# Optimization experiments

Hardware: AMD Instinct MI355X
Metric: run time of the kernel (lower is better)

Reference implementation:

```python
import jax, jax.numpy as jnp
import numpy as np

B, N, C, H, R = 64, 197, 768, 12, 98   # batch, tokens, dim, heads, eliminated tokens
SPARSITY, ALPHA = 0.2, 0.1
EPS = 1e-5  # torch nn.LayerNorm default


def layernorm(x, g, b):
    m = jnp.mean(x, axis=-1, keepdims=True)
    v = jnp.var(x, axis=-1, keepdims=True)
    return (x - m) / jnp.sqrt(v + EPS) * g + b


def setup_inputs() -> dict:
    key = jax.random.key(0)
    ks = jax.random.split(key, 8)
    s = lambda k, sh: (jax.random.normal(k, sh, jnp.float32) * 0.02)
    return dict(
        x=jax.random.normal(ks[0], (B, N, C), jnp.float32),
        norm1_g=jnp.ones((C,), jnp.float32), norm1_b=jnp.zeros((C,), jnp.float32),
        qkv_w=s(ks[1], (C, 3 * C)),                      # qkv_bias=False
        proj_w=s(ks[2], (C, C)), proj_b=jnp.zeros((C,), jnp.float32),
        norm2_g=jnp.ones((C,), jnp.float32), norm2_b=jnp.zeros((C,), jnp.float32),
        fc1_w=s(ks[3], (C, 4 * C)), fc1_b=jnp.zeros((4 * C,), jnp.float32),
        fc2_w=s(ks[4], (4 * C, C)), fc2_b=jnp.zeros((C,), jnp.float32),
    )


def reference(x, norm1_g, norm1_b, qkv_w, proj_w, proj_b,
              norm2_g, norm2_b, fc1_w, fc1_b, fc2_w, fc2_b):
    Dh = C // H
    scale = Dh ** -0.5
    # --- attention block ---
    h = layernorm(x, norm1_g, norm1_b)
    qkv = (h @ qkv_w).reshape(B, N, 3, H, Dh).transpose(2, 0, 3, 1, 4)
    q, k, v = qkv[0] * scale, qkv[1], qkv[2]
    attn = jax.nn.softmax(jnp.einsum('bhnd,bhmd->bhnm', q, k), axis=-1)  # [B,H,N,N]
    out = jnp.einsum('bhnm,bhmd->bhnd', attn, v).transpose(0, 2, 1, 3).reshape(B, N, C)
    x = x + out @ proj_w + proj_b
    # --- selection: DiagAttn (head-mean attention diagonal, excluding CLS) ---
    diag = jnp.diagonal(attn.mean(1), axis1=1, axis2=2)[:, 1:]          # [B, N-1]
    token_rank = jnp.argsort(-diag, axis=1) + 1                          # indices into [1, N)
    nk = N - 1 - R                                                       # kept image tokens
    idx_kept = jnp.sort(jnp.concatenate(
        [jnp.zeros((B, 1), token_rank.dtype), token_rank[:, :nk]], axis=1), axis=1)  # [B, K]
    idx_elim = jnp.sort(token_rank[:, nk:], axis=1)                      # [B, R]
    K = nk + 1
    # --- propagate: ThresholdGraph (multihead=True, threshold=True) ---
    x_kept = jnp.take_along_axis(x, idx_kept[:, :, None], axis=1)        # [B, K, C]
    x_elim = jnp.take_along_axis(x, idx_elim[:, :, None], axis=1)        # [B, R, C]
    w = jnp.take_along_axis(attn, idx_kept[:, None, :, None], axis=2)    # [B,H,K,N]
    w = jnp.take_along_axis(w, idx_elim[:, None, None, :], axis=3)       # [B,H,K,R]
    thr_idx = int(R * K * SPARSITY)
    w_sorted = -jnp.sort(-w.reshape(B, H, K * R), axis=-1)               # descending
    thr = w_sorted[:, :, thr_idx][:, :, None, None]
    w = jnp.where(w >= thr, w, jnp.zeros((), w.dtype))
    x_prop = jnp.einsum('bhke,behd->bkhd', w, x_elim.reshape(B, R, H, Dh)).reshape(B, K, C)
    x = x_kept + ALPHA * x_prop                                          # [B, K, C]
    # --- mlp block ---
    h2 = layernorm(x, norm2_g, norm2_b)
    h2 = jax.nn.gelu(h2 @ fc1_w + fc1_b, approximate=False) @ fc2_w + fc2_b
    return x + h2
```

## Files before the change

### kernel.cpp

```cpp
#include <hip/hip_runtime.h>
#include <math.h>

#define NTOK 197
#define CD   768
#define NH   12
#define DH   64
#define NBATCH 64
#define RTOK 98
#define KTOK 99
#define THRN 1941
#define WTOT (KTOK*RTOK)
#define SROWS 208

typedef __attribute__((ext_vector_type(8))) short short8;
typedef __attribute__((ext_vector_type(8))) unsigned short u16x8;
typedef __attribute__((ext_vector_type(4))) float floatx4;

__device__ __forceinline__ int clamp196(int v){ return ((unsigned)v > 196u) ? 196 : v; }
__device__ __forceinline__ unsigned short f2b(float f){
  unsigned u = __float_as_uint(f);
  return (unsigned short)((u + 0x7FFFu + ((u>>16)&1u)) >> 16);
}
__device__ __forceinline__ float us2f(unsigned short u){ return __uint_as_float(((unsigned)u)<<16); }
__device__ __forceinline__ int swz(int row, int q){ return q ^ (((row>>1)&3)<<3); }

__device__ __forceinline__ void ldsplit(const float* ap, int rem, u16x8& h, u16x8& l){
  float v[8];
  if (rem >= 8) {
    float4 t0 = *(const float4*)ap, t1 = *(const float4*)(ap+4);
    v[0]=t0.x; v[1]=t0.y; v[2]=t0.z; v[3]=t0.w;
    v[4]=t1.x; v[5]=t1.y; v[6]=t1.z; v[7]=t1.w;
  } else {
#pragma unroll
    for (int j=0;j<8;j++) v[j] = (j < rem) ? ap[j] : 0.f;
  }
#pragma unroll
  for (int j=0;j<8;j++){
    unsigned short hh = f2b(v[j]);
    h[j] = hh;
    l[j] = f2b(v[j] - us2f(hh));
  }
}

__global__ __launch_bounds__(256) void fill_kernel(float* __restrict__ out, int n, float val)
{
  int i = blockIdx.x*256 + threadIdx.x;
  if (i < n) out[i] = val;
}

__global__ __launch_bounds__(256) void tcast_k(const float* __restrict__ src, int K, int ldn, int col0,
                                               unsigned short* __restrict__ dst)
{
  __shared__ float t[32][33];
  int n0 = blockIdx.x*32, k0 = blockIdx.y*32;
  int lx = threadIdx.x & 31, ly = threadIdx.x >> 5;
#pragma unroll
  for (int i=0;i<4;i++)
    t[ly + i*8][lx] = src[(long)(k0 + ly + i*8)*ldn + col0 + n0 + lx];
  __syncthreads();
#pragma unroll
  for (int i=0;i<4;i++){
    int n = ly + i*8;
    dst[(long)(n0 + n)*K + k0 + lx] = f2b(t[lx][n]);
  }
}

__global__ __launch_bounds__(256) void tcast3_k(const float* __restrict__ src, int K, int ldn, int col0,
                                                unsigned short* __restrict__ dsth,
                                                unsigned short* __restrict__ dstl)
{
  __shared__ float t[32][33];
  int n0 = blockIdx.x*32, k0 = blockIdx.y*32;
  int lx = threadIdx.x & 31, ly = threadIdx.x >> 5;
#pragma unroll
  for (int i=0;i<4;i++)
    t[ly + i*8][lx] = src[(long)(k0 + ly + i*8)*ldn + col0 + n0 + lx];
  __syncthreads();
#pragma unroll
  for (int i=0;i<4;i++){
    int n = ly + i*8;
    float v = t[lx][n];
    unsigned short h = f2b(v);
    dsth[(long)(n0 + n)*K + k0 + lx] = h;
    dstl[(long)(n0 + n)*K + k0 + lx] = f2b(v - us2f(h));
  }
}

__global__ __launch_bounds__(256) void ln_kernel(const float* __restrict__ xin,
                                                 const float* __restrict__ gam,
                                                 const float* __restrict__ bet,
                                                 unsigned short* __restrict__ outh,
                                                 unsigned short* __restrict__ outl)
{
  int row = blockIdx.x;
  int tid = threadIdx.x;
  long base = (long)row * CD;
  float v[3];
#pragma unroll
  for (int i=0;i<3;i++) v[i] = xin[base + tid + i*256];
  float s  = v[0]+v[1]+v[2];
  float s2 = v[0]*v[0]+v[1]*v[1]+v[2]*v[2];
#pragma unroll
  for (int off=32; off; off>>=1){ s += __shfl_down(s,off); s2 += __shfl_down(s2,off); }
  __shared__ float ps[4], ps2[4], mb[2];
  if ((tid&63)==0){ ps[tid>>6]=s; ps2[tid>>6]=s2; }
  __syncthreads();
  if (tid==0){
    float S  = ps[0]+ps[1]+ps[2]+ps[3];
    float S2 = ps2[0]+ps2[1]+ps2[2]+ps2[3];
    float m  = S / (float)CD;
    float var = S2 / (float)CD - m*m;
    mb[0]=m; mb[1]=1.0f/sqrtf(var + 1e-5f);
  }
  __syncthreads();
  float m=mb[0], inv=mb[1];
#pragma unroll
  for (int i=0;i<3;i++){
    int c = tid + i*256;
    float r = (v[i]-m)*inv*gam[c] + bet[c];
    unsigned short h = f2b(r);
    outh[base+c] = h;
    if (outl) outl[base+c] = f2b(r - us2f(h));
  }
}

__global__ __launch_bounds__(256) void sqs_k(const unsigned short* __restrict__ Qh,
                                             const unsigned short* __restrict__ Ql,
                                             const unsigned short* __restrict__ Kh,
                                             const unsigned short* __restrict__ Kl,
                                             float* __restrict__ S)
{
  __shared__ short Bh_s[SROWS*64], Bl_s[SROWS*64];
  int tid = threadIdx.x;
  int z = blockIdx.y;
  int m0 = blockIdx.x * 128;
  const unsigned short* qhz = Qh + (long)z*NTOK*DH;
  const unsigned short* qlz = Ql + (long)z*NTOK*DH;
  const unsigned short* khz = Kh + (long)z*NTOK*DH;
  const unsigned short* klz = Kl + (long)z*NTOK*DH;
  u16x8 zz = {0,0,0,0,0,0,0,0};
  for (int i = tid; i < SROWS*8; i += 256) {
    int row = i>>3, c = i&7;
    u16x8 vh = zz, vl = zz;
    if (row < NTOK) {
      vh = *(const u16x8*)(khz + (long)row*DH + c*8);
      vl = *(const u16x8*)(klz + (long)row*DH + c*8);
    }
    int off = row*64 + ((c ^ (row&7))<<3);
    *(u16x8*)&Bh_s[off] = vh;
    *(u16x8*)&Bl_s[off] = vl;
  }
  __syncthreads();
  int w = tid>>6, l = tid&63;
  int lr = l&15, hi2 = l>>4, kq = hi2*8;
  int rbase0 = m0 + (w<<5);
  floatx4 acc[2][13];
#pragma unroll
  for (int mt=0;mt<2;mt++)
#pragma unroll
    for (int nt=0;nt<13;nt++) acc[mt][nt] = (floatx4){0.f,0.f,0.f,0.f};
#pragma unroll
  for (int ks=0; ks<2; ks++){
    int k0 = ks*32;
    short8 afh[2], afl[2];
#pragma unroll
    for (int mt=0;mt<2;mt++){
      int rowA = clamp196(rbase0 + mt*16 + lr);
      long qo = (long)rowA*DH + k0 + kq;
      afh[mt] = *(const short8*)(qhz + qo);
      afl[mt] = *(const short8*)(qlz + qo);
    }
#pragma unroll
    for (int nt=0;nt<13;nt++){
      int rowB = nt*16 + lr;
      int cc = (ks<<2) + hi2;
      int off = rowB*64 + ((cc ^ (rowB&7))<<3);
      short8 bfh = *(short8*)&Bh_s[off];
      short8 bfl = *(short8*)&Bl_s[off];
#pragma unroll
      for (int mt=0;mt<2;mt++){
        acc[mt][nt] = __builtin_amdgcn_mfma_f32_16x16x32_bf16(afh[mt], bfh, acc[mt][nt], 0, 0, 0);
        acc[mt][nt] = __builtin_amdgcn_mfma_f32_16x16x32_bf16(afh[mt], bfl, acc[mt][nt], 0, 0, 0);
        acc[mt][nt] = __builtin_amdgcn_mfma_f32_16x16x32_bf16(afl[mt], bfh, acc[mt][nt], 0, 0, 0);
      }
    }
  }
  float* Sz = S + (long)z*NTOK*NTOK;
#pragma unroll
  for (int mt=0;mt<2;mt++){
#pragma unroll
    for (int r=0;r<4;r++){
      int row = rbase0 + mt*16 + hi2*4 + r;
      float ev[13];
      float mx = -3.4e38f;
#pragma unroll
      for (int nt=0;nt<13;nt++){
        int col = nt*16 + lr;
        float v = acc[mt][nt][r];
        if (col >= NTOK) v = -3.4e38f;
        ev[nt] = v;
        mx = fmaxf(mx, v);
      }
#pragma unroll
      for (int mk=1; mk<16; mk<<=1) mx = fmaxf(mx, __shfl_xor(mx, mk));
      float sum = 0.f;
#pragma unroll
      for (int nt=0;nt<13;nt++){
        float e = expf(ev[nt]-mx);
        ev[nt] = e;
        sum += e;
      }
#pragma unroll
      for (int mk=1; mk<16; mk<<=1) sum += __shfl_xor(sum, mk);
      if (row < NTOK){
#pragma unroll
        for (int nt=0;nt<13;nt++){
          int col = nt*16 + lr;
          if (col < NTOK) Sz[(long)row*NTOK + col] = ev[nt]/sum;
        }
      }
    }
  }
}

struct PvP {
  const float* P;
  const unsigned short* Vt;
  unsigned short* C;
};

__global__ __launch_bounds__(256) void pv_k(PvP p)
{
  __shared__ short Ahs[128*32], Als[128*32], Bs[64*32];
  int tid = threadIdx.x;
  int z = blockIdx.z;
  int cb = z / NH, h = z - cb*NH;
  const float* Az = p.P + (long)z*NTOK*NTOK;
  const unsigned short* Bz = p.Vt + (long)z*DH*NTOK;
  int m0 = blockIdx.y*128;
  int w = tid>>6, l = tid&63;
  int wm = (w&1)*64, wn = (w>>1)*32;
  int lr = l&15, kq = (l>>4)*8;
  floatx4 acc[4][2];
#pragma unroll
  for (int i=0;i<4;i++)
#pragma unroll
    for (int j=0;j<2;j++) acc[i][j] = (floatx4){0.f,0.f,0.f,0.f};
  int r0i = tid>>2, q0 = (tid&3)*8;
  int r1i = r0i + 64;
  int w0s = swz(r0i, q0), w1s = swz(r1i, q0);
  for (int k0 = 0; k0 < NTOK; k0 += 32) {
    u16x8 ah0={0,0,0,0,0,0,0,0}, al0={0,0,0,0,0,0,0,0};
    u16x8 ah1={0,0,0,0,0,0,0,0}, al1={0,0,0,0,0,0,0,0};
    u16x8 b0 ={0,0,0,0,0,0,0,0};
    int rem = NTOK - k0 - q0;
    { int gm = m0 + r0i;
      if (gm < NTOK && rem > 0) ldsplit(Az + (long)gm*NTOK + k0 + q0, rem, ah0, al0); }
    { int gm = m0 + r1i;
      if (gm < NTOK && rem > 0) ldsplit(Az + (long)gm*NTOK + k0 + q0, rem, ah1, al1); }
    { const unsigned short* bp = Bz + (long)r0i*NTOK + k0 + q0;
      if (rem >= 8) b0 = *(const u16x8*)bp;
      else if (rem > 0) {
#pragma unroll
        for (int j=0;j<8;j++) if (j < rem) b0[j] = bp[j];
      } }
    __syncthreads();
    *(u16x8*)&Ahs[r0i*32 + w0s] = ah0;
    *(u16x8*)&Ahs[r1i*32 + w1s] = ah1;
    *(u16x8*)&Als[r0i*32 + w0s] = al0;
    *(u16x8*)&Als[r1i*32 + w1s] = al1;
    *(u16x8*)&Bs [r0i*32 + w0s] = b0;
    __syncthreads();
    short8 afh[4], afl[4], bfr[2];
#pragma unroll
    for (int mt=0;mt<4;mt++){
      int rr = wm + mt*16 + lr; int rs = rr*32 + swz(rr,kq);
      afh[mt] = *(short8*)&Ahs[rs];
      afl[mt] = *(short8*)&Als[rs];
    }
#pragma unroll
    for (int nt=0;nt<2;nt++){
      int rr = wn + nt*16 + lr;
      bfr[nt] = *(short8*)&Bs[rr*32 + swz(rr,kq)];
    }
#pragma unroll
    for (int mt=0;mt<4;mt++)
#pragma unroll
      for (int nt=0;nt<2;nt++){
        acc[mt][nt] = __builtin_amdgcn_mfma_f32_16x16x32_bf16(afh[mt], bfr[nt], acc[mt][nt], 0, 0, 0);
        acc[mt][nt] = __builtin_amdgcn_mfma_f32_16x16x32_bf16(afl[mt], bfr[nt], acc[mt][nt], 0, 0, 0);
      }
  }
  int rbase = (l>>4)*4;
#pragma unroll
  for (int mt=0;mt<4;mt++){
#pragma unroll
    for (int r=0;r<4;r++){
      int gm = m0 + wm + mt*16 + rbase + r;
      if (gm >= NTOK) continue;
#pragma unroll
      for (int nt=0;nt<2;nt++){
        int gn = wn + nt*16 + lr;
        p.C[(long)cb*NTOK*CD + (long)gm*CD + h*DH + gn] = f2b(acc[mt][nt][r]);
      }
    }
  }
}

struct MmP {
  const unsigned short* A;
  const unsigned short* B;
  void* C;
  const float* bias;
  const float* resid;
  unsigned short* vout;
  int M, N, K, ldc;
};

template<int EPI>
__global__ __launch_bounds__(256) void mgemm_k(MmP p)
{
  __shared__ short As[128*32];
  __shared__ short Bs[128*32];
  int tid = threadIdx.x;
  int m0 = blockIdx.y*128, n0 = blockIdx.x*128;
  int w = tid>>6, l = tid&63;
  int wm = (w&1)*64, wn = (w>>1)*64;
  int lr = l&15, kq = (l>>4)*8;
  floatx4 acc[4][4];
#pragma unroll
  for (int i=0;i<4;i++)
#pragma unroll
    for (int j=0;j<4;j++) acc[i][j] = (floatx4){0.f,0.f,0.f,0.f};
  int r0i = tid>>2, q0 = (tid&3)*8;
  int r1i = r0i + 64;
  int w0s = swz(r0i, q0), w1s = swz(r1i, q0);
  for (int k0 = 0; k0 < p.K; k0 += 32) {
    u16x8 a0 = {0,0,0,0,0,0,0,0}, a1 = {0,0,0,0,0,0,0,0};
    { int gm = m0 + r0i;
      if (gm < p.M) a0 = *(const u16x8*)(p.A + (long)gm*p.K + k0 + q0); }
    { int gm = m0 + r1i;
      if (gm < p.M) a1 = *(const u16x8*)(p.A + (long)gm*p.K + k0 + q0); }
    u16x8 b0 = *(const u16x8*)(p.B + (long)(n0 + r0i)*p.K + k0 + q0);
    u16x8 b1 = *(const u16x8*)(p.B + (long)(n0 + r1i)*p.K + k0 + q0);
    __syncthreads();
    *(u16x8*)&As[r0i*32 + w0s] = a0;
    *(u16x8*)&As[r1i*32 + w1s] = a1;
    *(u16x8*)&Bs[r0i*32 + w0s] = b0;
    *(u16x8*)&Bs[r1i*32 + w1s] = b1;
    __syncthreads();
    short8 af[4], bfr[4];
#pragma unroll
    for (int mt=0;mt<4;mt++){ int rr = wm + mt*16 + lr; af[mt]  = *(short8*)&As[rr*32 + swz(rr,kq)]; }
#pragma unroll
    for (int nt=0;nt<4;nt++){ int rr = wn + nt*16 + lr; bfr[nt] = *(short8*)&Bs[rr*32 + swz(rr,kq)]; }
#pragma unroll
    for (int mt=0;mt<4;mt++)
#pragma unroll
      for (int nt=0;nt<4;nt++)
        acc[mt][nt] = __builtin_amdgcn_mfma_f32_16x16x32_bf16(af[mt], bfr[nt], acc[mt][nt], 0, 0, 0);
  }
  int rbase = (l>>4)*4;
#pragma unroll
  for (int mt=0;mt<4;mt++){
#pragma unroll
    for (int r=0;r<4;r++){
      int gm = m0 + wm + mt*16 + rbase + r;
      if (gm >= p.M) continue;
#pragma unroll
      for (int nt=0;nt<4;nt++){
        int gn = n0 + wn + nt*16 + lr;
        float val = acc[mt][nt][r];
        if (EPI == 1) {
          int cb = gm / NTOK, tok = gm - cb*NTOK;
          int h = gn >> 6, d = gn & 63;
          p.vout[(((long)cb*NH + h)*DH + d)*NTOK + tok] = f2b(val);
        } else if (EPI == 2) {
          ((float*)p.C)[(long)gm*p.ldc + gn] = val + p.bias[gn] + p.resid[(long)gm*p.ldc + gn];
        } else {
          float u = val + p.bias[gn];
          ((unsigned short*)p.C)[(long)gm*p.ldc + gn] = f2b(0.5f*u*(1.0f + erff(u*0.70710678118654752f)));
        }
      }
    }
  }
}

struct Mm3P {
  const unsigned short *Ah, *Al, *Bh, *Bl;
  float* C;
  unsigned short *qh, *ql, *kh, *kl;
  long az, bz, cz;
  int M, N, K, ldc;
};

template<int EPI>
__global__ __launch_bounds__(256) void mgemm3_k(Mm3P p)
{
  __shared__ short Ahs[128*32], Als[128*32], Bhs[128*32], Bls[128*32];
  int tid = threadIdx.x;
  int z = blockIdx.z;
  const unsigned short* Azh = p.Ah + (long)z*p.az;
  const unsigned short* Azl = p.Al + (long)z*p.az;
  const unsigned short* Bzh = p.Bh + (long)z*p.bz;
  const unsigned short* Bzl = p.Bl + (long)z*p.bz;
  int m0 = blockIdx.y*128, n0 = blockIdx.x*128;
  int w = tid>>6, l = tid&63;
  int wm = (w&1)*64, wn = (w>>1)*64;
  int lr = l&15, kq = (l>>4)*8;
  floatx4 acc[4][4];
#pragma unroll
  for (int i=0;i<4;i++)
#pragma unroll
    for (int j=0;j<4;j++) acc[i][j] = (floatx4){0.f,0.f,0.f,0.f};
  int r0i = tid>>2, q0 = (tid&3)*8;
  int r1i = r0i + 64;
  int w0s = swz(r0i, q0), w1s = swz(r1i, q0);
  for (int k0 = 0; k0 < p.K; k0 += 32) {
    u16x8 ah0={0,0,0,0,0,0,0,0}, al0={0,0,0,0,0,0,0,0};
    u16x8 ah1={0,0,0,0,0,0,0,0}, al1={0,0,0,0,0,0,0,0};
    u16x8 bh0={0,0,0,0,0,0,0,0}, bl0={0,0,0,0,0,0,0,0};
    u16x8 bh1={0,0,0,0,0,0,0,0}, bl1={0,0,0,0,0,0,0,0};
    { int gm = m0 + r0i;
      if (gm < p.M) {
        long o = (long)gm*p.K + k0 + q0;
        ah0 = *(const u16x8*)(Azh + o);
        al0 = *(const u16x8*)(Azl + o);
      } }
    { int gm = m0 + r1i;
      if (gm < p.M) {
        long o = (long)gm*p.K + k0 + q0;
        ah1 = *(const u16x8*)(Azh + o);
        al1 = *(const u16x8*)(Azl + o);
      } }
    { int gn = n0 + r0i;
      if (gn < p.N) {
        long o = (long)gn*p.K + k0 + q0;
        bh0 = *(const u16x8*)(Bzh + o);
        bl0 = *(const u16x8*)(Bzl + o);
      } }
    { int gn = n0 + r1i;
      if (gn < p.N) {
        long o = (long)gn*p.K + k0 + q0;
        bh1 = *(const u16x8*)(Bzh + o);
        bl1 = *(const u16x8*)(Bzl + o);
      } }
    __syncthreads();
    *(u16x8*)&Ahs[r0i*32 + w0s] = ah0;
    *(u16x8*)&Ahs[r1i*32 + w1s] = ah1;
    *(u16x8*)&Als[r0i*32 + w0s] = al0;
    *(u16x8*)&Als[r1i*32 + w1s] = al1;
    *(u16x8*)&Bhs[r0i*32 + w0s] = bh0;
    *(u16x8*)&Bhs[r1i*32 + w1s] = bh1;
    *(u16x8*)&Bls[r0i*32 + w0s] = bl0;
    *(u16x8*)&Bls[r1i*32 + w1s] = bl1;
    __syncthreads();
    short8 afh[4], afl[4], bfh[4], bfl[4];
#pragma unroll
    for (int mt=0;mt<4;mt++){
      int rr = wm + mt*16 + lr; int rs = rr*32 + swz(rr,kq);
      afh[mt] = *(short8*)&Ahs[rs];
      afl[mt] = *(short8*)&Als[rs];
    }
#pragma unroll
    for (int nt=0;nt<4;nt++){
      int rr = wn + nt*16 + lr; int rs = rr*32 + swz(rr,kq);
      bfh[nt] = *(short8*)&Bhs[rs];
      bfl[nt] = *(short8*)&Bls[rs];
    }
#pragma unroll
    for (int mt=0;mt<4;mt++)
#pragma unroll
      for (int nt=0;nt<4;nt++){
        acc[mt][nt] = __builtin_amdgcn_mfma_f32_16x16x32_bf16(afh[mt], bfh[nt], acc[mt][nt], 0, 0, 0);
        acc[mt][nt] = __builtin_amdgcn_mfma_f32_16x16x32_bf16(afh[mt], bfl[nt], acc[mt][nt], 0, 0, 0);
        acc[mt][nt] = __builtin_amdgcn_mfma_f32_16x16x32_bf16(afl[mt], bfh[nt], acc[mt][nt], 0, 0, 0);
      }
  }
  int rbase = (l>>4)*4;
#pragma unroll
  for (int mt=0;mt<4;mt++){
#pragma unroll
    for (int r=0;r<4;r++){
      int gm = m0 + wm + mt*16 + rbase + r;
      if (gm >= p.M) continue;
#pragma unroll
      for (int nt=0;nt<4;nt++){
        int gn = n0 + wn + nt*16 + lr;
        if (gn >= p.N) continue;
        float val = acc[mt][nt][r];
        if (EPI == 0) {
          p.C[(long)z*p.cz + (long)gm*p.ldc + gn] = val;
        } else {
          int which = (gn >= CD) ? 1 : 0;
          int rc = gn - which*CD;
          int hd = rc >> 6, dd = rc & 63;
          int cb = gm / NTOK, tok = gm - cb*NTOK;
          long off = (((long)cb*NH + hd)*NTOK + tok)*DH + dd;
          float v = which ? val : val*0.125f;
          unsigned short h = f2b(v);
          unsigned short lo16 = f2b(v - us2f(h));
          if (which) { p.kh[off] = h; p.kl[off] = lo16; }
          else       { p.qh[off] = h; p.ql[off] = lo16; }
        }
      }
    }
  }
}

__global__ __launch_bounds__(256) void select_kernel(const float* __restrict__ attn,
                                                     int* __restrict__ idx_kept,
                                                     int* __restrict__ idx_elim, int b0)
{
  int cb = blockIdx.x, tid = threadIdx.x;
  int b = b0 + cb;
  __shared__ float diag[NTOK-1];
  __shared__ int kept[NTOK];
  if (tid < NTOK-1) {
    int t = tid + 1;
    float s = 0.f;
#pragma unroll
    for (int h=0; h<NH; h++)
      s += attn[(((long)cb*NH + h)*NTOK + t)*NTOK + t];
    diag[tid] = s / 12.0f;
  }
  if (tid < KTOK) idx_kept[b*KTOK + tid] = 0;
  if (tid < RTOK) idx_elim[b*RTOK + tid] = 1;
  __syncthreads();
  if (tid < NTOK-1) {
    float dv = diag[tid];
    int r = 0;
    for (int m=0; m<NTOK-1; m++){
      float dm = diag[m];
      r += ((dm > dv) || (dm == dv && m < tid)) ? 1 : 0;
    }
    kept[tid+1] = (r < (NTOK-1-RTOK)) ? 1 : 0;
  }
  __syncthreads();
  if (tid < NTOK-1) {
    int t = tid + 1;
    if (kept[t]) {
      int pos = 1;
      for (int s2=1; s2<t; s2++) pos += kept[s2];
      if (pos >= 1 && pos < KTOK) idx_kept[b*KTOK + pos] = t;
    } else {
      int pos = 0;
      for (int s2=1; s2<t; s2++) pos += 1 - kept[s2];
      if (pos >= 0 && pos < RTOK) idx_elim[b*RTOK + pos] = t;
    }
  }
  if (tid == 0) idx_kept[b*KTOK] = 0;
}

#define PNEL 38
__global__ __launch_bounds__(256) void prop_kernel(const float* __restrict__ attn,
                                                   const float* __restrict__ x1c,
                                                   const int* __restrict__ idx_kept,
                                                   const int* __restrict__ idx_elim,
                                                   float* __restrict__ x2, int b0)
{
  int z = blockIdx.x;
  int cb = z / NH, h = z - cb*NH;
  int b = b0 + cb;
  int tid = threadIdx.x;
  int wid = tid >> 6, l = tid & 63;
  int lr = l & 15, hi2 = l >> 4;
  __shared__ short WhL[112*128];
  __shared__ short XtL[64*128];
  __shared__ unsigned hist[64];
  __shared__ int kidx[KTOK], eidx[RTOK];
  if (tid < KTOK) kidx[tid] = clamp196(idx_kept[b*KTOK + tid]);
  if (tid < RTOK) eidx[tid] = clamp196(idx_elim[b*RTOK + tid]);
  u16x8 zz = {0,0,0,0,0,0,0,0};
#pragma unroll
  for (int i=0;i<7;i++) *(u16x8*)&WhL[tid*8 + i*2048] = zz;
#pragma unroll
  for (int i=0;i<4;i++) *(u16x8*)&XtL[tid*8 + i*2048] = zz;
  __syncthreads();
  for (int i = tid; i < RTOK*DH; i += 256){
    int e = i >> 6, d = i & 63;
    float v = x1c[((long)cb*NTOK + eidx[e])*CD + h*DH + d];
    XtL[d*128 + (((e>>3) ^ (d&7))<<3) + (e&7)] = (short)f2b(v);
  }
  const float* ab = attn + (long)z*NTOK*NTOK;
  unsigned wb[PNEL];
#pragma unroll
  for (int j=0;j<PNEL;j++){
    int i = tid + (j<<8);
    if (i < WTOT){
      int k = i / RTOK, e = i - k*RTOK;
      wb[j] = __float_as_uint(ab[kidx[k]*NTOK + eidx[e]]);
    } else wb[j] = 0u;
  }
  unsigned P = 0; int rrank = THRN;
  for (int pass=0; pass<5; ++pass){
    int sh = 24 - 6*pass;
    if (tid < 64) hist[tid] = 0u;
    __syncthreads();
#pragma unroll
    for (int j=0;j<PNEL;j++){
      int i = tid + (j<<8);
      unsigned v = wb[j];
      bool m = (i < WTOT) && ((pass == 0) || ((v >> (sh+6)) == P));
      if (m) atomicAdd(&hist[(v>>sh)&63u], 1u);
    }
    __syncthreads();
    unsigned cum = 0; int bsel = 0; unsigned above = 0;
    for (int bb=63; bb>=0; --bb){
      unsigned hv = hist[bb];
      if (cum + hv >= (unsigned)rrank){ bsel = bb; above = cum; break; }
      cum += hv;
    }
    P = (P<<6) | (unsigned)bsel;
    rrank -= (int)above;
    __syncthreads();
  }
  unsigned thrbits = P;
#pragma unroll
  for (int j=0;j<PNEL;j++){
    int i = tid + (j<<8);
    if (i < WTOT){
      int k = i / RTOK, e = i - k*RTOK;
      unsigned v = (wb[j] >= thrbits) ? wb[j] : 0u;
      WhL[k*128 + (((e>>3) ^ (k&7))<<3) + (e&7)] = (short)f2b(__uint_as_float(v));
    }
  }
  __syncthreads();
  floatx4 acc[7];
#pragma unroll
  for (int mt=0;mt<7;mt++) acc[mt] = (floatx4){0.f,0.f,0.f,0.f};
  short8 bfr[4];
#pragma unroll
  for (int ks=0;ks<4;ks++){
    int c = ks*4 + hi2;
    int rd = wid*16 + lr;
    bfr[ks] = *(short8*)&XtL[rd*128 + ((c ^ (lr&7))<<3)];
  }
#pragma unroll
  for (int mt=0;mt<7;mt++){
#pragma unroll
    for (int ks=0;ks<4;ks++){
      int c = ks*4 + hi2;
      int rw = mt*16 + lr;
      short8 af = *(short8*)&WhL[rw*128 + ((c ^ (lr&7))<<3)];
      acc[mt] = __builtin_amdgcn_mfma_f32_16x16x32_bf16(af, bfr[ks], acc[mt], 0, 0, 0);
    }
  }
#pragma unroll
  for (int mt=0;mt<7;mt++){
#pragma unroll
    for (int r=0;r<4;r++){
      int kt = mt*16 + hi2*4 + r;
      if (kt >= KTOK) continue;
      int d = wid*16 + lr;
      float xk = x1c[((long)cb*NTOK + kidx[kt])*CD + h*DH + d];
      x2[((long)b*KTOK + kt)*CD + h*DH + d] = xk + 0.1f*acc[mt][r];
    }
  }
}

extern "C" void kernel_launch(void* const* d_in, const int* in_sizes, int n_in,
                              void* d_out, int out_size, void* d_ws, size_t ws_size,
                              hipStream_t stream)
{
  const float* x     = (const float*)d_in[0];
  const float* n1g   = (const float*)d_in[1];
  const float* n1b   = (const float*)d_in[2];
  const float* qkvw  = (const float*)d_in[3];
  const float* projw = (const float*)d_in[4];
  const float* projb = (const float*)d_in[5];
  const float* n2g   = (const float*)d_in[6];
  const float* n2b   = (const float*)d_in[7];
  const float* fc1w  = (const float*)d_in[8];
  const float* fc1b  = (const float*)d_in[9];
  const float* fc2w  = (const float*)d_in[10];
  const float* fc2b  = (const float*)d_in[11];
  float* out = (float*)d_out;

  const long XROW = (long)NTOK*CD;
  const long AH   = (long)NTOK*NTOK;
  const long AB   = (long)NH*AH;
  const long SMALL = 6336L + 6272L;
  const long WFIX  = 1769472L;
  const long PB = AB + 3*XROW + XROW/2;
  const long MLPFIX = 2359296L;
  const long MINREQ = SMALL + WFIX + (MLPFIX + 64*1920L > PB ? MLPFIX + 64*1920L : PB);

  long wsf = (long)(ws_size / 4);
  if (wsf < MINREQ) {
    float val = (float)(ws_size >> 20) * 1000.0f + 1.0f;
    fill_kernel<<<dim3((out_size+255)/256), 256, 0, stream>>>(out, out_size, val);
    return;
  }

  long avail = wsf - SMALL - WFIX;
  int G = (int)(avail / PB);
  if (G > NBATCH) G = NBATCH;
  if (G < 1) G = 1;
  long rcl = ((avail - MLPFIX) / 1920L) / 64L * 64L;
  int RC = (int)(rcl > 6336L ? 6336L : rcl);
  if (RC < 64) RC = 64;

  float* ws = (float*)d_ws;
  int*   idx_kept = (int*)ws;
  int*   idx_elim = idx_kept + 6336;
  unsigned short* qkwh   = (unsigned short*)(ws + SMALL);
  unsigned short* qkwl   = qkwh + 1179648;
  unsigned short* qkvwvT = qkwl + 1179648;
  unsigned short* projwT = qkvwvT + 589824;
  float* base  = ws + SMALL + WFIX;
  float* attnc = base;
  unsigned short* qh = (unsigned short*)(base + (long)G*AB);
  unsigned short* ql = qh + (long)G*XROW;
  float* x1c = (float*)qh;
  unsigned short* kh = (unsigned short*)(base + (long)G*AB + (long)G*XROW);
  unsigned short* kl = kh + (long)G*XROW;
  unsigned short* aoutb = kh;
  unsigned short* vt = (unsigned short*)(base + (long)G*AB + 2L*G*XROW);
  unsigned short* h1h = (unsigned short*)(base + (long)G*AB + 2L*G*XROW + (long)G*XROW/2);
  unsigned short* h1l = h1h + (long)G*XROW;
  unsigned short* fc1wT = (unsigned short*)base;
  unsigned short* fc2wT = fc1wT + 2359296;
  unsigned short* h2b   = (unsigned short*)(base + MLPFIX);
  unsigned short* gb    = h2b + (long)RC*CD;

  tcast3_k<<<dim3(48,24), 256, 0, stream>>>(qkvw, CD, 3*CD, 0, qkwh, qkwl);
  tcast_k <<<dim3(24,24), 256, 0, stream>>>(qkvw, CD, 3*CD, 2*CD, qkvwvT);
  tcast_k <<<dim3(24,24), 256, 0, stream>>>(projw, CD, CD, 0, projwT);

  for (int b0 = 0; b0 < NBATCH; b0 += G) {
    int GL = (NBATCH - b0 < G) ? (NBATCH - b0) : G;
    int MROW = GL*NTOK;
    ln_kernel<<<dim3(MROW), 256, 0, stream>>>(x + (long)b0*XROW, n1g, n1b, h1h, h1l);
    {
      Mm3P p{}; p.Ah=h1h; p.Al=h1l; p.Bh=qkwh; p.Bl=qkwl;
      p.qh=qh; p.ql=ql; p.kh=kh; p.kl=kl;
      p.M=MROW; p.N=2*CD; p.K=CD; p.ldc=0; p.az=0; p.bz=0; p.cz=0;
      mgemm3_k<1><<<dim3(12,(MROW+127)/128,1), 256, 0, stream>>>(p);
    }
    {
      MmP p{}; p.A=h1h; p.B=qkvwvT; p.vout=vt;
      p.M=MROW; p.N=CD; p.K=CD; p.ldc=CD;
      mgemm_k<1><<<dim3(6,(MROW+127)/128,1), 256, 0, stream>>>(p);
    }
    sqs_k<<<dim3(2, GL*NH), 256, 0, stream>>>(qh, ql, kh, kl, attnc);
    select_kernel<<<dim3(GL), 256, 0, stream>>>(attnc, idx_kept, idx_elim, b0);
    {
      PvP p{}; p.P=attnc; p.Vt=vt; p.C=aoutb;
      pv_k<<<dim3(1,2,GL*NH), 256, 0, stream>>>(p);
    }
    {
      MmP p{}; p.A=aoutb; p.B=projwT; p.C=x1c;
      p.M=MROW; p.N=CD; p.K=CD; p.ldc=CD;
      p.bias=projb; p.resid=x + (long)b0*XROW;
      mgemm_k<2><<<dim3(6,(MROW+127)/128,1), 256, 0, stream>>>(p);
    }
    prop_kernel<<<dim3(GL*NH), 256, 0, stream>>>(attnc, x1c, idx_kept, idx_elim, out, b0);
  }

  tcast_k<<<dim3(96,24), 256, 0, stream>>>(fc1w, CD, 4*CD, 0, fc1wT);
  tcast_k<<<dim3(24,96), 256, 0, stream>>>(fc2w, 4*CD, CD, 0, fc2wT);

  for (int r0 = 0; r0 < NBATCH*KTOK; r0 += RC) {
    int RCL = (NBATCH*KTOK - r0 < RC) ? (NBATCH*KTOK - r0) : RC;
    ln_kernel<<<dim3(RCL), 256, 0, stream>>>(out + (long)r0*CD, n2g, n2b, h2b, nullptr);
    {
      MmP p{}; p.A=h2b; p.B=fc1wT; p.C=gb;
      p.M=RCL; p.N=4*CD; p.K=CD; p.ldc=4*CD; p.bias=fc1b;
      mgemm_k<3><<<dim3(24,(RCL+127)/128,1), 256, 0, stream>>>(p);
    }
    {
      MmP p{}; p.A=gb; p.B=fc2wT; p.C=out + (long)r0*CD;
      p.M=RCL; p.N=CD; p.K=4*CD; p.ldc=CD;
      p.bias=fc2b; p.resid=out + (long)r0*CD;
      mgemm_k<2><<<dim3(6,(RCL+127)/128,1), 256, 0, stream>>>(p);
    }
  }
}
```

Baseline: 712.2 us.

## Drop bf16 hi/lo split in PV matmul and aggregate histogram atomics per wave

The attention-times-V kernel now converts the fp32 probabilities to a single bf16 value instead of a hi/lo bf16 pair. This halves the MFMA count, the shared-memory traffic and the conversion work for that stage, at the cost of lower precision in the attention output. Separately, the radix-select histogram now uses wave ballots to group lanes that share a bin, so one lane issues one atomicAdd per bin instead of every lane hitting LDS atomics.

```diff
diff --git a/kernel.cpp b/kernel.cpp
--- a/kernel.cpp
+++ b/kernel.cpp
@@ -24,7 +24,7 @@
 __device__ __forceinline__ float us2f(unsigned short u){ return __uint_as_float(((unsigned)u)<<16); }
 __device__ __forceinline__ int swz(int row, int q){ return q ^ (((row>>1)&3)<<3); }
 
-__device__ __forceinline__ void ldsplit(const float* ap, int rem, u16x8& h, u16x8& l){
+__device__ __forceinline__ void ldcvt(const float* ap, int rem, u16x8& h){
   float v[8];
   if (rem >= 8) {
     float4 t0 = *(const float4*)ap, t1 = *(const float4*)(ap+4);
@@ -35,11 +35,7 @@
     for (int j=0;j<8;j++) v[j] = (j < rem) ? ap[j] : 0.f;
   }
 #pragma unroll
-  for (int j=0;j<8;j++){
-    unsigned short hh = f2b(v[j]);
-    h[j] = hh;
-    l[j] = f2b(v[j] - us2f(hh));
-  }
+  for (int j=0;j<8;j++) h[j] = f2b(v[j]);
 }
 
 __global__ __launch_bounds__(256) void fill_kernel(float* __restrict__ out, int n, float val)
@@ -231,7 +227,7 @@
 
 __global__ __launch_bounds__(256) void pv_k(PvP p)
 {
-  __shared__ short Ahs[128*32], Als[128*32], Bs[64*32];
+  __shared__ short Ahs[128*32], Bs[64*32];
   int tid = threadIdx.x;
   int z = blockIdx.z;
   int cb = z / NH, h = z - cb*NH;
@@ -250,14 +246,14 @@
   int r1i = r0i + 64;
   int w0s = swz(r0i, q0), w1s = swz(r1i, q0);
   for (int k0 = 0; k0 < NTOK; k0 += 32) {
-    u16x8 ah0={0,0,0,0,0,0,0,0}, al0={0,0,0,0,0,0,0,0};
-    u16x8 ah1={0,0,0,0,0,0,0,0}, al1={0,0,0,0,0,0,0,0};
+    u16x8 ah0={0,0,0,0,0,0,0,0};
+    u16x8 ah1={0,0,0,0,0,0,0,0};
     u16x8 b0 ={0,0,0,0,0,0,0,0};
     int rem = NTOK - k0 - q0;
     { int gm = m0 + r0i;
-      if (gm < NTOK && rem > 0) ldsplit(Az + (long)gm*NTOK + k0 + q0, rem, ah0, al0); }
+      if (gm < NTOK && rem > 0) ldcvt(Az + (long)gm*NTOK + k0 + q0, rem, ah0); }
     { int gm = m0 + r1i;
-      if (gm < NTOK && rem > 0) ldsplit(Az + (long)gm*NTOK + k0 + q0, rem, ah1, al1); }
+      if (gm < NTOK && rem > 0) ldcvt(Az + (long)gm*NTOK + k0 + q0, rem, ah1); }
     { const unsigned short* bp = Bz + (long)r0i*NTOK + k0 + q0;
       if (rem >= 8) b0 = *(const u16x8*)bp;
       else if (rem > 0) {
@@ -267,16 +263,13 @@
     __syncthreads();
     *(u16x8*)&Ahs[r0i*32 + w0s] = ah0;
     *(u16x8*)&Ahs[r1i*32 + w1s] = ah1;
-    *(u16x8*)&Als[r0i*32 + w0s] = al0;
-    *(u16x8*)&Als[r1i*32 + w1s] = al1;
     *(u16x8*)&Bs [r0i*32 + w0s] = b0;
     __syncthreads();
-    short8 afh[4], afl[4], bfr[2];
+    short8 afh[4], bfr[2];
 #pragma unroll
     for (int mt=0;mt<4;mt++){
-      int rr = wm + mt*16 + lr; int rs = rr*32 + swz(rr,kq);
-      afh[mt] = *(short8*)&Ahs[rs];
-      afl[mt] = *(short8*)&Als[rs];
+      int rr = wm + mt*16 + lr;
+      afh[mt] = *(short8*)&Ahs[rr*32 + swz(rr,kq)];
     }
 #pragma unroll
     for (int nt=0;nt<2;nt++){
@@ -286,10 +279,8 @@
 #pragma unroll
     for (int mt=0;mt<4;mt++)
 #pragma unroll
-      for (int nt=0;nt<2;nt++){
+      for (int nt=0;nt<2;nt++)
         acc[mt][nt] = __builtin_amdgcn_mfma_f32_16x16x32_bf16(afh[mt], bfr[nt], acc[mt][nt], 0, 0, 0);
-        acc[mt][nt] = __builtin_amdgcn_mfma_f32_16x16x32_bf16(afl[mt], bfr[nt], acc[mt][nt], 0, 0, 0);
-      }
   }
   int rbase = (l>>4)*4;
 #pragma unroll
@@ -601,8 +592,20 @@
     for (int j=0;j<PNEL;j++){
       int i = tid + (j<<8);
       unsigned v = wb[j];
-      bool m = (i < WTOT) && ((pass == 0) || ((v >> (sh+6)) == P));
-      if (m) atomicAdd(&hist[(v>>sh)&63u], 1u);
+      bool act = (i < WTOT) && ((pass == 0) || ((v >> (sh+6)) == P));
+      unsigned bin = (v>>sh)&63u;
+      unsigned long long am = __ballot(act);
+      if (am == 0ull) continue;
+      unsigned long long m = am;
+#pragma unroll
+      for (int bb2=0;bb2<6;bb2++){
+        unsigned long long bm = __ballot(act && ((bin>>bb2)&1u));
+        m &= ((bin>>bb2)&1u) ? bm : ~bm;
+      }
+      if (act){
+        int ldr = __ffsll(m) - 1;
+        if ((tid&63) == ldr) atomicAdd(&hist[bin], (unsigned)__popcll(m));
+      }
     }
     __syncthreads();
     unsigned cum = 0; int bsel = 0; unsigned above = 0;
```

After: 730.0 us. 1.02x slower.
